# Performance work log

Hardware: AMD Instinct MI355X
Metric: run time of the kernel (lower is better)

## Reference

```python
import jax, jax.numpy as jnp
import numpy as np

N, H, O, E = 32768, 512, 512, 16


def setup_inputs() -> dict:
    key = jax.random.key(0)
    k0, k1, k2 = jax.random.split(key, 3)
    x = jax.random.normal(k0, (N, H), dtype=jnp.float32)
    # gate Linear(H -> E)
    Wg = jax.random.normal(k1, (E, H), dtype=jnp.float32) * (1.0 / np.sqrt(H))
    bg = jnp.zeros((E,), dtype=jnp.float32)
    # expert Linears(H -> O), stacked [E, O, H]
    We = jax.random.normal(k2, (E, O, H), dtype=jnp.float32) * (1.0 / np.sqrt(H))
    be = jnp.zeros((E, O), dtype=jnp.float32)
    return {"x": x, "Wg": Wg, "bg": bg, "We": We, "be": be}


def reference(x, Wg, bg, We, be):
    # gate: softmax over experts, then top-1 (argmax)
    logits = x @ Wg.T + bg                       # [N, E]
    weights = jax.nn.softmax(logits, axis=-1)
    expert_idx = jnp.argmax(weights, axis=-1)    # [N]
    # run every expert on every token, then select the top-1 expert's output.
    # (note: original module does NOT scale output by the gate weight)
    all_out = jnp.einsum('nh,eoh->neo', x, We) + be[None]   # [N, E, O]
    out = jnp.take_along_axis(all_out, expert_idx[:, None, None], axis=1)[:, 0]  # [N, O]
    return out
```

## Files before the change

kernel.cpp:

```cpp
#include <hip/hip_runtime.h>
#include <hip/hip_bf16.h>
#include <stdint.h>

#define NTOK 32768
#define HDIM 512
#define ODIM 512
#define NEXP 16

#define TM 128
#define TN 128
#define BK 32
#define MTILES 32

#define CSTRIDE 32

typedef __bf16 bf16x8 __attribute__((ext_vector_type(8)));
typedef float  floatx4 __attribute__((ext_vector_type(4)));

__device__ __forceinline__ unsigned pk2(unsigned lo, unsigned hi) {
  return (lo >> 16) | (hi & 0xffff0000u);
}

__device__ __forceinline__ bf16x8 asbf8(uint4 u) { bf16x8 v; __builtin_memcpy(&v, &u, 16); return v; }

__device__ __forceinline__ void split3(float4 a, float4 b, uint4* H, uint4* M, uint4* L) {
  float f[8] = {a.x, a.y, a.z, a.w, b.x, b.y, b.z, b.w};
  unsigned h[8], m[8], l[8];
#pragma unroll
  for (int j = 0; j < 8; ++j) {
    union { float F; unsigned U; } u; u.F = f[j];
    h[j] = u.U & 0xffff0000u;
    union { unsigned U; float F; } hv; hv.U = h[j];
    float r1 = f[j] - hv.F;
    union { float F; unsigned U; } r1u; r1u.F = r1;
    m[j] = r1u.U & 0xffff0000u;
    union { unsigned U; float F; } mv; mv.U = m[j];
    float r2 = r1 - mv.F;
    union { float F; unsigned U; } r2u; r2u.F = r2;
    l[j] = r2u.U;
  }
  H->x = pk2(h[0], h[1]); H->y = pk2(h[2], h[3]); H->z = pk2(h[4], h[5]); H->w = pk2(h[6], h[7]);
  M->x = pk2(m[0], m[1]); M->y = pk2(m[2], m[3]); M->z = pk2(m[4], m[5]); M->w = pk2(m[6], m[7]);
  L->x = pk2(l[0], l[1]); L->y = pk2(l[2], l[3]); L->z = pk2(l[4], l[5]); L->w = pk2(l[6], l[7]);
}

#define GLDS16(g, l) __builtin_amdgcn_global_load_lds( \
    (const __attribute__((address_space(1))) unsigned int*)(g), \
    (__attribute__((address_space(3))) unsigned int*)(l), 16, 0, 0)

__global__ __launch_bounds__(256) void cvt_we_kernel(const float* __restrict__ We,
                                                     unsigned short* __restrict__ out) {
  int i = blockIdx.x * 256 + threadIdx.x;
  const float4* src = (const float4*)We;
  float4 a = src[2 * i];
  float4 b = src[2 * i + 1];
  union { float F; unsigned U; } t[8] = {{a.x},{a.y},{a.z},{a.w},{b.x},{b.y},{b.z},{b.w}};
  uint4 o;
  o.x = pk2(t[0].U, t[1].U); o.y = pk2(t[2].U, t[3].U);
  o.z = pk2(t[4].U, t[5].U); o.w = pk2(t[6].U, t[7].U);
  ((uint4*)out)[i] = o;
}

__global__ __launch_bounds__(256, 2) void gate_kernel(const float* __restrict__ x,
                                                      const float* __restrict__ Wg,
                                                      const float* __restrict__ bg,
                                                      int* __restrict__ counts,
                                                      int* __restrict__ buckets,
                                                      unsigned short* __restrict__ xbf) {
  __shared__ __align__(16) unsigned short whf[16][64][8];
  __shared__ __align__(16) unsigned short wmf[16][64][8];
  __shared__ __align__(16) unsigned short wlf[16][64][8];
  __shared__ __align__(16) float red[4][4][16][20];

  int t = threadIdx.x;
  int lane = t & 63;
  int w = t >> 6;
  int tok0 = blockIdx.x * 64;

#pragma unroll
  for (int q = 0; q < 4; ++q) {
    int id = q * 256 + t;
    int s = id >> 6;
    int l = id & 63;
    const float* src = Wg + (size_t)(l & 15) * HDIM + s * 32 + (l >> 4) * 8;
    float4 a = *(const float4*)src;
    float4 b = *(const float4*)(src + 4);
    uint4 H, M, L;
    split3(a, b, &H, &M, &L);
    *(uint4*)&whf[s][l][0] = H;
    *(uint4*)&wmf[s][l][0] = M;
    *(uint4*)&wlf[s][l][0] = L;
  }
  __syncthreads();

  int fr = lane & 15;
  int quad = lane >> 4;
  floatx4 acc[4] = {};

  const float* xbase[4];
#pragma unroll
  for (int mt = 0; mt < 4; ++mt)
    xbase[mt] = x + (size_t)(tok0 + mt * 16 + fr) * HDIM + (w * 4) * 32 + quad * 8;

  float4 xa[4], xb[4];
#pragma unroll
  for (int mt = 0; mt < 4; ++mt) {
    xa[mt] = *(const float4*)(xbase[mt]);
    xb[mt] = *(const float4*)(xbase[mt] + 4);
  }

#pragma unroll
  for (int si = 0; si < 4; ++si) {
    int s = w * 4 + si;
    bf16x8 bh = *(const bf16x8*)&whf[s][lane][0];
    bf16x8 bm = *(const bf16x8*)&wmf[s][lane][0];
    bf16x8 bl = *(const bf16x8*)&wlf[s][lane][0];
    float4 na[4], nb[4];
    if (si < 3) {
#pragma unroll
      for (int mt = 0; mt < 4; ++mt) {
        na[mt] = *(const float4*)(xbase[mt] + (si + 1) * 32);
        nb[mt] = *(const float4*)(xbase[mt] + (si + 1) * 32 + 4);
      }
    }
#pragma unroll
    for (int mt = 0; mt < 4; ++mt) {
      size_t row = tok0 + mt * 16 + fr;
      uint4 H, M, L;
      split3(xa[mt], xb[mt], &H, &M, &L);
      *(uint4*)(xbf + row * HDIM + s * 32 + quad * 8) = H;
      bf16x8 ah = asbf8(H), am = asbf8(M), al = asbf8(L);
      acc[mt] = __builtin_amdgcn_mfma_f32_16x16x32_bf16(ah, bh, acc[mt], 0, 0, 0);
      acc[mt] = __builtin_amdgcn_mfma_f32_16x16x32_bf16(ah, bm, acc[mt], 0, 0, 0);
      acc[mt] = __builtin_amdgcn_mfma_f32_16x16x32_bf16(am, bh, acc[mt], 0, 0, 0);
      acc[mt] = __builtin_amdgcn_mfma_f32_16x16x32_bf16(am, bm, acc[mt], 0, 0, 0);
      acc[mt] = __builtin_amdgcn_mfma_f32_16x16x32_bf16(ah, bl, acc[mt], 0, 0, 0);
      acc[mt] = __builtin_amdgcn_mfma_f32_16x16x32_bf16(al, bh, acc[mt], 0, 0, 0);
      acc[mt] = __builtin_amdgcn_mfma_f32_16x16x32_bf16(am, bl, acc[mt], 0, 0, 0);
      acc[mt] = __builtin_amdgcn_mfma_f32_16x16x32_bf16(al, bm, acc[mt], 0, 0, 0);
    }
    if (si < 3) {
#pragma unroll
      for (int mt = 0; mt < 4; ++mt) { xa[mt] = na[mt]; xb[mt] = nb[mt]; }
    }
  }

#pragma unroll
  for (int mt = 0; mt < 4; ++mt)
#pragma unroll
    for (int i = 0; i < 4; ++i)
      red[w][mt][quad * 4 + i][fr] = acc[mt][i];
  __syncthreads();

  if (t < 64) {
    int tk = t;
    int mt = tk >> 4;
    int r = tk & 15;
    float4 tot4[4];
#pragma unroll
    for (int eq = 0; eq < 4; ++eq) tot4[eq] = *(const float4*)&bg[eq * 4];
#pragma unroll
    for (int ww = 0; ww < 4; ++ww)
#pragma unroll
      for (int eq = 0; eq < 4; ++eq) {
        float4 v = *(const float4*)&red[ww][mt][r][eq * 4];
        tot4[eq].x += v.x; tot4[eq].y += v.y; tot4[eq].z += v.z; tot4[eq].w += v.w;
      }
    float tot[16];
#pragma unroll
    for (int eq = 0; eq < 4; ++eq) {
      tot[eq * 4 + 0] = tot4[eq].x; tot[eq * 4 + 1] = tot4[eq].y;
      tot[eq * 4 + 2] = tot4[eq].z; tot[eq * 4 + 3] = tot4[eq].w;
    }
    float bv = tot[0]; int bi = 0;
#pragma unroll
    for (int e = 1; e < NEXP; ++e) if (tot[e] > bv) { bv = tot[e]; bi = e; }

    int token = tok0 + tk;
    for (int ee = 0; ee < NEXP; ++ee) {
      int e = (ee + blockIdx.x) & 15;
      unsigned long long mask = __ballot(bi == e);
      if (mask) {
        int leader = __builtin_ctzll(mask);
        int base = 0;
        if (lane == leader) base = atomicAdd(&counts[e << 5], (int)__popcll(mask));
        base = __shfl(base, leader, 64);
        if (bi == e) {
          int rank = (int)__popcll(mask & ((1ull << lane) - 1ull));
          buckets[e * NTOK + base + rank] = token;
        }
      }
    }
  }
}

__global__ __launch_bounds__(256, 4) void moe_gemm(const unsigned short* __restrict__ xbf,
                                                   const unsigned short* __restrict__ webf,
                                                   const float* __restrict__ be,
                                                   const int* __restrict__ counts,
                                                   const int* __restrict__ buckets,
                                                   float* __restrict__ out) {
  int e = blockIdx.z;
  int cnt = counts[e << 5];
  int m0 = blockIdx.x * TM;
  if (m0 >= cnt) return;
  int o0 = blockIdx.y * TN;

  __shared__ __align__(16) unsigned short As[2][TM * BK];
  __shared__ __align__(16) unsigned short Bs[2][TN * BK];
  __shared__ int toks[TM];

  int t = threadIdx.x;
  int lane = t & 63;
  int w = t >> 6;

  if (t < TM) {
    int r = m0 + t;
    toks[t] = (r < cnt) ? buckets[e * NTOK + r] : buckets[e * NTOK];
  }
  __syncthreads();

  int pl = lane >> 3;
  int sl = lane & 7;
  int slog = sl ^ pl;
  int rsub = 2 * pl + (slog >> 2);
  int cch = slog & 3;
  const unsigned short* agp[2];
  const unsigned short* bgp[2];
#pragma unroll
  for (int j = 0; j < 2; ++j) {
    int row = w * 32 + j * 16 + rsub;
    agp[j] = xbf + (size_t)toks[row] * HDIM + cch * 8;
    bgp[j] = webf + ((size_t)e * ODIM + o0 + row) * HDIM + cch * 8;
  }

  int wm = (w & 1) * 64;
  int wn = (w >> 1) * 64;
  int fr = lane & 15;
  int quad = lane >> 4;

  int aoff[4], boff[4];
#pragma unroll
  for (int mt = 0; mt < 4; ++mt) {
    int m = wm + mt * 16 + fr;
    int pr = m >> 1;
    aoff[mt] = pr * 64 + (((((m & 1) << 2) | quad) ^ (pr & 7)) << 3);
    int n = wn + mt * 16 + fr;
    int pn = n >> 1;
    boff[mt] = pn * 64 + (((((n & 1) << 2) | quad) ^ (pn & 7)) << 3);
  }

  float bias[4];
#pragma unroll
  for (int nt = 0; nt < 4; ++nt)
    bias[nt] = be[e * ODIM + o0 + wn + nt * 16 + fr];

  floatx4 acc[4][4] = {};

  int dst = w * 1024;

#pragma unroll
  for (int j = 0; j < 2; ++j) {
    GLDS16(agp[j], As[0] + dst + j * 512);
    GLDS16(bgp[j], Bs[0] + dst + j * 512);
  }

  for (int k = 0; k < HDIM / BK; ++k) {
    int p = k & 1;
    __syncthreads();
    if (k < HDIM / BK - 1) {
      int koff = (k + 1) * BK;
#pragma unroll
      for (int j = 0; j < 2; ++j) {
        GLDS16(agp[j] + koff, As[1 - p] + dst + j * 512);
        GLDS16(bgp[j] + koff, Bs[1 - p] + dst + j * 512);
      }
    }

    bf16x8 af[4], bfr[4];
#pragma unroll
    for (int mt = 0; mt < 4; ++mt)
      af[mt] = *(const bf16x8*)(As[p] + aoff[mt]);
#pragma unroll
    for (int nt = 0; nt < 4; ++nt)
      bfr[nt] = *(const bf16x8*)(Bs[p] + boff[nt]);
#pragma unroll
    for (int mt = 0; mt < 4; ++mt)
#pragma unroll
      for (int nt = 0; nt < 4; ++nt)
        acc[mt][nt] = __builtin_amdgcn_mfma_f32_16x16x32_bf16(af[mt], bfr[nt], acc[mt][nt], 0, 0, 0);
  }

  int rbase = wm + quad * 4;
#pragma unroll
  for (int nt = 0; nt < 4; ++nt) {
    int col = o0 + wn + nt * 16 + fr;
#pragma unroll
    for (int mt = 0; mt < 4; ++mt) {
#pragma unroll
      for (int i = 0; i < 4; ++i) {
        int rl = rbase + mt * 16 + i;
        if (m0 + rl < cnt) {
          out[(size_t)toks[rl] * ODIM + col] = acc[mt][nt][i] + bias[nt];
        }
      }
    }
  }
}

#define WS_BUCKETS 4096
#define WS_XBF (WS_BUCKETS + NEXP * NTOK * 4)
#define WS_WEBF (WS_XBF + NTOK * HDIM * 2)

extern "C" void kernel_launch(void* const* d_in, const int* in_sizes, int n_in,
                              void* d_out, int out_size, void* d_ws, size_t ws_size,
                              hipStream_t stream) {
  const float* x  = (const float*)d_in[0];
  const float* Wg = (const float*)d_in[1];
  const float* bg = (const float*)d_in[2];
  const float* We = (const float*)d_in[3];
  const float* be = (const float*)d_in[4];
  float* out = (float*)d_out;
  char* ws = (char*)d_ws;

  int* counts = (int*)ws;
  int* buckets = (int*)(ws + WS_BUCKETS);
  unsigned short* xbf  = (unsigned short*)(ws + WS_XBF);
  unsigned short* webf = (unsigned short*)(ws + WS_WEBF);

  hipMemsetAsync(counts, 0, NEXP * CSTRIDE * 4, stream);
  cvt_we_kernel<<<NEXP * ODIM * HDIM / 8 / 256, 256, 0, stream>>>(We, webf);
  gate_kernel<<<NTOK / 64, 256, 0, stream>>>(x, Wg, bg, counts, buckets, xbf);
  moe_gemm<<<dim3(MTILES, ODIM / TN, NEXP), 256, 0, stream>>>(xbf, webf, be, counts, buckets, out);
}
```

Measured before the change: 202.6 us.

## Triple-buffer LDS in MoE GEMM with explicit vmcnt waits and barriers

Replaces the double-buffered K loop with a three-stage LDS pipeline that prefetches two tiles ahead. It uses manual s_waitcnt vmcnt and raw s_barrier with sched_barrier fences, so the wait no longer drains every outstanding load. The bias load moves to after the loop to cut live registers, and the occupancy hint drops from 4 to 3 blocks per CU to make room for the larger LDS footprint. The risks are lower occupancy and correctness that depends on the hand-written vmcnt counts matching the issued loads.

```diff
diff --git a/kernel.cpp b/kernel.cpp
--- a/kernel.cpp
+++ b/kernel.cpp
@@ -194,7 +194,7 @@
   }
 }
 
-__global__ __launch_bounds__(256, 4) void moe_gemm(const unsigned short* __restrict__ xbf,
+__global__ __launch_bounds__(256, 3) void moe_gemm(const unsigned short* __restrict__ xbf,
                                                    const unsigned short* __restrict__ webf,
                                                    const float* __restrict__ be,
                                                    const int* __restrict__ counts,
@@ -206,8 +206,8 @@
   if (m0 >= cnt) return;
   int o0 = blockIdx.y * TN;
 
-  __shared__ __align__(16) unsigned short As[2][TM * BK];
-  __shared__ __align__(16) unsigned short Bs[2][TN * BK];
+  __shared__ __align__(16) unsigned short As[3][TM * BK];
+  __shared__ __align__(16) unsigned short Bs[3][TN * BK];
   __shared__ int toks[TM];
 
   int t = threadIdx.x;
@@ -250,11 +250,6 @@
     boff[mt] = pn * 64 + (((((n & 1) << 2) | quad) ^ (pn & 7)) << 3);
   }
 
-  float bias[4];
-#pragma unroll
-  for (int nt = 0; nt < 4; ++nt)
-    bias[nt] = be[e * ODIM + o0 + wn + nt * 16 + fr];
-
   floatx4 acc[4][4] = {};
 
   int dst = w * 1024;
@@ -264,32 +259,54 @@
     GLDS16(agp[j], As[0] + dst + j * 512);
     GLDS16(bgp[j], Bs[0] + dst + j * 512);
   }
-
-  for (int k = 0; k < HDIM / BK; ++k) {
-    int p = k & 1;
-    __syncthreads();
-    if (k < HDIM / BK - 1) {
-      int koff = (k + 1) * BK;
+#pragma unroll
+  for (int j = 0; j < 2; ++j) {
+    GLDS16(agp[j] + BK, As[1] + dst + j * 512);
+    GLDS16(bgp[j] + BK, Bs[1] + dst + j * 512);
+  }
+
+  const int NK = HDIM / BK;
+#pragma unroll
+  for (int k = 0; k < NK; ++k) {
+    __builtin_amdgcn_sched_barrier(0);
+    if (k < NK - 1) {
+      asm volatile("s_waitcnt vmcnt(4)" ::: "memory");
+    } else {
+      asm volatile("s_waitcnt vmcnt(0)" ::: "memory");
+    }
+    __builtin_amdgcn_s_barrier();
+    __builtin_amdgcn_sched_barrier(0);
+
+    if (k + 2 < NK) {
+      int b2 = (k + 2) % 3;
+      int koff = (k + 2) * BK;
 #pragma unroll
       for (int j = 0; j < 2; ++j) {
-        GLDS16(agp[j] + koff, As[1 - p] + dst + j * 512);
-        GLDS16(bgp[j] + koff, Bs[1 - p] + dst + j * 512);
-      }
-    }
-
+        GLDS16(agp[j] + koff, As[b2] + dst + j * 512);
+        GLDS16(bgp[j] + koff, Bs[b2] + dst + j * 512);
+      }
+    }
+
+    int b = k % 3;
     bf16x8 af[4], bfr[4];
 #pragma unroll
     for (int mt = 0; mt < 4; ++mt)
-      af[mt] = *(const bf16x8*)(As[p] + aoff[mt]);
+      af[mt] = *(const bf16x8*)(As[b] + aoff[mt]);
 #pragma unroll
     for (int nt = 0; nt < 4; ++nt)
-      bfr[nt] = *(const bf16x8*)(Bs[p] + boff[nt]);
+      bfr[nt] = *(const bf16x8*)(Bs[b] + boff[nt]);
 #pragma unroll
     for (int mt = 0; mt < 4; ++mt)
 #pragma unroll
       for (int nt = 0; nt < 4; ++nt)
         acc[mt][nt] = __builtin_amdgcn_mfma_f32_16x16x32_bf16(af[mt], bfr[nt], acc[mt][nt], 0, 0, 0);
   }
+  __builtin_amdgcn_sched_barrier(0);
+
+  float bias[4];
+#pragma unroll
+  for (int nt = 0; nt < 4; ++nt)
+    bias[nt] = be[e * ODIM + o0 + wn + nt * 16 + fr];
 
   int rbase = wm + quad * 4;
 #pragma unroll
@@ -328,7 +345,7 @@
   unsigned short* xbf  = (unsigned short*)(ws + WS_XBF);
   unsigned short* webf = (unsigned short*)(ws + WS_WEBF);
 
-  hipMemsetAsync(counts, 0, NEXP * CSTRIDE * 4, stream);
+  (void)hipMemsetAsync(counts, 0, NEXP * CSTRIDE * 4, stream);
   cvt_we_kernel<<<NEXP * ODIM * HDIM / 8 / 256, 256, 0, stream>>>(We, webf);
   gate_kernel<<<NTOK / 64, 256, 0, stream>>>(x, Wg, bg, counts, buckets, xbf);
   moe_gemm<<<dim3(MTILES, ODIM / TN, NEXP), 256, 0, stream>>>(xbf, webf, be, counts, buckets, out);
```

Result: slower. 212.2 us (+4.8%).

## Fuse expert weight bf16 conversion into GEMM B-tile loads

Applied to the files above, without the earlier changes.

Drops the separate kernel that converted the expert weights to bf16. The GEMM now reads fp32 weights straight into registers, truncates them to bf16 and writes them into the swizzled LDS tile for the next stage, with the store placed after the MFMAs. This removes one launch and the write and re-read of the 8 MB bf16 copy. In exchange every GEMM block reads fp32 weights, twice the bytes per tile, and converts them repeatedly across the token tiles, with register-staged loads in place of direct-to-LDS loads.

```diff
diff --git a/kernel.cpp b/kernel.cpp
--- a/kernel.cpp
+++ b/kernel.cpp
@@ -19,6 +19,10 @@
 
 __device__ __forceinline__ unsigned pk2(unsigned lo, unsigned hi) {
   return (lo >> 16) | (hi & 0xffff0000u);
+}
+
+__device__ __forceinline__ unsigned fbits(float f) {
+  union { float F; unsigned U; } u; u.F = f; return u.U;
 }
 
 __device__ __forceinline__ bf16x8 asbf8(uint4 u) { bf16x8 v; __builtin_memcpy(&v, &u, 16); return v; }
@@ -47,19 +51,6 @@
 #define GLDS16(g, l) __builtin_amdgcn_global_load_lds( \
     (const __attribute__((address_space(1))) unsigned int*)(g), \
     (__attribute__((address_space(3))) unsigned int*)(l), 16, 0, 0)
-
-__global__ __launch_bounds__(256) void cvt_we_kernel(const float* __restrict__ We,
-                                                     unsigned short* __restrict__ out) {
-  int i = blockIdx.x * 256 + threadIdx.x;
-  const float4* src = (const float4*)We;
-  float4 a = src[2 * i];
-  float4 b = src[2 * i + 1];
-  union { float F; unsigned U; } t[8] = {{a.x},{a.y},{a.z},{a.w},{b.x},{b.y},{b.z},{b.w}};
-  uint4 o;
-  o.x = pk2(t[0].U, t[1].U); o.y = pk2(t[2].U, t[3].U);
-  o.z = pk2(t[4].U, t[5].U); o.w = pk2(t[6].U, t[7].U);
-  ((uint4*)out)[i] = o;
-}
 
 __global__ __launch_bounds__(256, 2) void gate_kernel(const float* __restrict__ x,
                                                       const float* __restrict__ Wg,
@@ -195,7 +186,7 @@
 }
 
 __global__ __launch_bounds__(256, 4) void moe_gemm(const unsigned short* __restrict__ xbf,
-                                                   const unsigned short* __restrict__ webf,
+                                                   const float* __restrict__ We,
                                                    const float* __restrict__ be,
                                                    const int* __restrict__ counts,
                                                    const int* __restrict__ buckets,
@@ -226,13 +217,20 @@
   int rsub = 2 * pl + (slog >> 2);
   int cch = slog & 3;
   const unsigned short* agp[2];
-  const unsigned short* bgp[2];
 #pragma unroll
   for (int j = 0; j < 2; ++j) {
     int row = w * 32 + j * 16 + rsub;
     agp[j] = xbf + (size_t)toks[row] * HDIM + cch * 8;
-    bgp[j] = webf + ((size_t)e * ODIM + o0 + row) * HDIM + cch * 8;
-  }
+  }
+
+  int br5 = lane >> 1;
+  int bh = lane & 1;
+  const float* wgp = We + ((size_t)e * ODIM + o0 + w * 32 + br5) * HDIM + bh * 16;
+  int bpair = w * 16 + (lane >> 2);
+  int brb = br5 & 1;
+  int bslot0 = (((brb << 2) | (bh << 1))) ^ ((lane >> 2) & 7);
+  int bwo0 = bpair * 64 + bslot0 * 8;
+  int bwo1 = bpair * 64 + (bslot0 ^ 1) * 8;
 
   int wm = (w & 1) * 64;
   int wn = (w >> 1) * 64;
@@ -260,23 +258,43 @@
   int dst = w * 1024;
 
 #pragma unroll
-  for (int j = 0; j < 2; ++j) {
+  for (int j = 0; j < 2; ++j)
     GLDS16(agp[j], As[0] + dst + j * 512);
-    GLDS16(bgp[j], Bs[0] + dst + j * 512);
+  {
+    float4 v0 = *(const float4*)(wgp + 0);
+    float4 v1 = *(const float4*)(wgp + 4);
+    float4 v2 = *(const float4*)(wgp + 8);
+    float4 v3 = *(const float4*)(wgp + 12);
+    uint4 q0, q1;
+    q0.x = pk2(fbits(v0.x), fbits(v0.y)); q0.y = pk2(fbits(v0.z), fbits(v0.w));
+    q0.z = pk2(fbits(v1.x), fbits(v1.y)); q0.w = pk2(fbits(v1.z), fbits(v1.w));
+    q1.x = pk2(fbits(v2.x), fbits(v2.y)); q1.y = pk2(fbits(v2.z), fbits(v2.w));
+    q1.z = pk2(fbits(v3.x), fbits(v3.y)); q1.w = pk2(fbits(v3.z), fbits(v3.w));
+    *(uint4*)(Bs[0] + bwo0) = q0;
+    *(uint4*)(Bs[0] + bwo1) = q1;
   }
 
   for (int k = 0; k < HDIM / BK; ++k) {
     int p = k & 1;
     __syncthreads();
+    float4 v0, v1, v2, v3;
     if (k < HDIM / BK - 1) {
       int koff = (k + 1) * BK;
 #pragma unroll
-      for (int j = 0; j < 2; ++j) {
+      for (int j = 0; j < 2; ++j)
         GLDS16(agp[j] + koff, As[1 - p] + dst + j * 512);
-        GLDS16(bgp[j] + koff, Bs[1 - p] + dst + j * 512);
-      }
-    }
-
+      const float* wp = wgp + koff;
+      v0 = *(const float4*)(wp + 0);
+      v1 = *(const float4*)(wp + 4);
+      v2 = *(const float4*)(wp + 8);
+      v3 = *(const float4*)(wp + 12);
+    }
+
+#pragma unroll
+    for (int kk = 0; kk < 2; ++kk) {
+      int cb = kk * 4 + quad;
+      (void)cb;
+    }
     bf16x8 af[4], bfr[4];
 #pragma unroll
     for (int mt = 0; mt < 4; ++mt)
@@ -289,6 +307,16 @@
 #pragma unroll
       for (int nt = 0; nt < 4; ++nt)
         acc[mt][nt] = __builtin_amdgcn_mfma_f32_16x16x32_bf16(af[mt], bfr[nt], acc[mt][nt], 0, 0, 0);
+
+    if (k < HDIM / BK - 1) {
+      uint4 q0, q1;
+      q0.x = pk2(fbits(v0.x), fbits(v0.y)); q0.y = pk2(fbits(v0.z), fbits(v0.w));
+      q0.z = pk2(fbits(v1.x), fbits(v1.y)); q0.w = pk2(fbits(v1.z), fbits(v1.w));
+      q1.x = pk2(fbits(v2.x), fbits(v2.y)); q1.y = pk2(fbits(v2.z), fbits(v2.w));
+      q1.z = pk2(fbits(v3.x), fbits(v3.y)); q1.w = pk2(fbits(v3.z), fbits(v3.w));
+      *(uint4*)(Bs[1 - p] + bwo0) = q0;
+      *(uint4*)(Bs[1 - p] + bwo1) = q1;
+    }
   }
 
   int rbase = wm + quad * 4;
@@ -310,7 +338,6 @@
 
 #define WS_BUCKETS 4096
 #define WS_XBF (WS_BUCKETS + NEXP * NTOK * 4)
-#define WS_WEBF (WS_XBF + NTOK * HDIM * 2)
 
 extern "C" void kernel_launch(void* const* d_in, const int* in_sizes, int n_in,
                               void* d_out, int out_size, void* d_ws, size_t ws_size,
@@ -325,11 +352,9 @@
 
   int* counts = (int*)ws;
   int* buckets = (int*)(ws + WS_BUCKETS);
-  unsigned short* xbf  = (unsigned short*)(ws + WS_XBF);
-  unsigned short* webf = (unsigned short*)(ws + WS_WEBF);
-
-  hipMemsetAsync(counts, 0, NEXP * CSTRIDE * 4, stream);
-  cvt_we_kernel<<<NEXP * ODIM * HDIM / 8 / 256, 256, 0, stream>>>(We, webf);
+  unsigned short* xbf = (unsigned short*)(ws + WS_XBF);
+
+  (void)hipMemsetAsync(counts, 0, NEXP * CSTRIDE * 4, stream);
   gate_kernel<<<NTOK / 64, 256, 0, stream>>>(x, Wg, bg, counts, buckets, xbf);
-  moe_gemm<<<dim3(MTILES, ODIM / TN, NEXP), 256, 0, stream>>>(xbf, webf, be, counts, buckets, out);
-}
+  moe_gemm<<<dim3(MTILES, ODIM / TN, NEXP), 256, 0, stream>>>(xbf, We, be, counts, buckets, out);
+}
```

Result: slower. 222.0 us (+9.6%).
